# Performance work log

Hardware: AMD Instinct MI355X
Metric: run time of the kernel (lower is better)

## Reference

```python
import jax, jax.numpy as jnp
import numpy as np

B = 8192          # graphs
A = 1024          # atoms per graph
F = 32            # max fragments per graph
N = B * A
VIRTUAL_IDX = 4   # HPARAMS.get_node_idx('ligand_virtual')


def setup_inputs() -> dict:
    key = jax.random.key(0)
    k1, k2, k3, k4 = jax.random.split(key, 4)
    pos = jax.random.normal(k1, (N, 3), dtype=jnp.float32) * 10.0
    # -1 marks non-ligand atoms (no fragment), as in frag_idx_map semantics
    frag_idx_map = jax.random.randint(k2, (N,), -1, F, dtype=jnp.int32)
    batch_idx = (jnp.arange(N, dtype=jnp.int32) // A).astype(jnp.int32)
    node_entity = jax.random.randint(k3, (N,), 0, 6, dtype=jnp.int32)
    mask = jax.random.bernoulli(k4, 0.95, (N,))
    return {"pos": pos, "frag_idx_map": frag_idx_map, "batch_idx": batch_idx,
            "node_entity": node_entity, "mask": mask,
            "num_graphs": B, "max_frags_per_graph": F}


def reference(pos, frag_idx_map, batch_idx, node_entity, mask,
              num_graphs, max_frags_per_graph):
    """Fused equivalent of get_flat_fragment_index + get_fragment_com.

    Returns (coms [B*F, 3], counts [B*F], flat_frag_idx [N]).
    Rows of coms beyond a graph's actual fragment count are zero-padded.
    """
    Bn = num_graphs
    Fm = max_frags_per_graph
    is_ligand = frag_idx_map >= 0

    # num_frags_per_graph[i] = max(frag_idx in graph i) + 1 (0 if none)
    fmax = jax.ops.segment_max(jnp.where(is_ligand, frag_idx_map, -1),
                               batch_idx, num_segments=Bn)
    nfrag = jnp.maximum(fmax, -1) + 1  # [B]
    offset = jnp.concatenate([jnp.zeros((1,), nfrag.dtype),
                              jnp.cumsum(nfrag)[:-1]])  # [B]

    # flat fragment index in [0, sum(F_i)), -1 for non-ligand atoms
    flat_frag_idx = jnp.where(is_ligand,
                              frag_idx_map + offset[batch_idx],
                              -1)

    # COM excludes virtual nodes and masked dummies
    valid = is_ligand & mask & (node_entity != VIRTUAL_IDX)
    n_seg = Bn * Fm
    seg = jnp.where(valid, flat_frag_idx, n_seg)  # dump invalid into trash segment
    w = valid.astype(pos.dtype)
    sums = jax.ops.segment_sum(pos * w[:, None], seg, num_segments=n_seg + 1)[:-1]
    cnt = jax.ops.segment_sum(w, seg, num_segments=n_seg + 1)[:-1]
    coms = sums / jnp.maximum(cnt, 1.0)[:, None]
    return coms, cnt, flat_frag_idx
```

## Files before the change

kernel.cpp:

```cpp
#include <hip/hip_runtime.h>

#define GA 1024
#define GF 32
#define VIRT 4

typedef _Float16 half8 __attribute__((ext_vector_type(8)));
typedef float f32x4 __attribute__((ext_vector_type(4)));
typedef unsigned int uint4v __attribute__((ext_vector_type(4)));

#define XSTRIDE 2080
#define KOFF    (4 * XSTRIDE)
#define FOFF    (KOFF + GA)
#define LDSSZ   (FOFF + 4 * GF * 4 * 4)

__device__ __forceinline__ unsigned int h2(float a, float b) {
    const unsigned short lo = __builtin_bit_cast(unsigned short, (_Float16)a);
    const unsigned short hi = __builtin_bit_cast(unsigned short, (_Float16)b);
    return (unsigned int)lo | ((unsigned int)hi << 16);
}

__global__ __launch_bounds__(256) void k_graph_acc(
    const float* __restrict__ pos,
    const int*   __restrict__ frag,
    const int*   __restrict__ entity,
    const int*   __restrict__ mask,
    float*       __restrict__ sums_cnt,
    int*         __restrict__ nfrag)
{
    const int g    = blockIdx.x;
    const int t    = threadIdx.x;
    const int lane = t & 63;
    const int w    = t >> 6;

    __shared__ alignas(16) unsigned char lds[LDSSZ];
    __shared__ int s_wmax[4];

    const int i0 = g * GA + t * 4;
    const int4  f4 = *(const int4*)(frag   + i0);
    const int4  e4 = *(const int4*)(entity + i0);
    const int4  m4 = *(const int4*)(mask   + i0);
    const float4* p4 = (const float4*)(pos + (size_t)3 * i0);
    const float4 pa = p4[0], pb = p4[1], pc = p4[2];

    #define KEY(F,M,E) ((unsigned)(((F) >= 0 && (M) != 0 && (E) != VIRT) ? (unsigned)(F) : 0xFFu))
    const unsigned kp = KEY(f4.x,m4.x,e4.x)        | (KEY(f4.y,m4.y,e4.y) << 8)
                      | (KEY(f4.z,m4.z,e4.z) << 16) | (KEY(f4.w,m4.w,e4.w) << 24);
    *(unsigned*)(lds + KOFF + t * 4) = kp;
    #undef KEY

    *(uint2*)(lds + 0 * XSTRIDE + t * 8) = make_uint2(h2(pa.x, pa.w), h2(pb.z, pc.y));
    *(uint2*)(lds + 1 * XSTRIDE + t * 8) = make_uint2(h2(pa.y, pb.x), h2(pb.w, pc.z));
    *(uint2*)(lds + 2 * XSTRIDE + t * 8) = make_uint2(h2(pa.z, pb.y), h2(pc.x, pc.w));
    *(uint2*)(lds + 3 * XSTRIDE + t * 8) = make_uint2(0x3C003C00u, 0x3C003C00u);

    int lm = max(max(f4.x, f4.y), max(f4.z, f4.w));
    #pragma unroll
    for (int off = 32; off > 0; off >>= 1)
        lm = max(lm, __shfl_down(lm, off, 64));
    if (lane == 0) s_wmax[w] = lm;

    f32x4 acc0 = {0.f, 0.f, 0.f, 0.f};
    f32x4 acc1 = {0.f, 0.f, 0.f, 0.f};
    const int row = lane & 15;
    const int grp = lane >> 4;
    const unsigned xoff = (unsigned)((row & 3) * XSTRIDE + (w * 256 + grp * 8) * 2);
    const unsigned koff = (unsigned)(KOFF + w * 256 + grp * 8);

    #pragma unroll
    for (int s = 0; s < 8; ++s) {
        const uint2  kk = *(const uint2*)(lds + koff + s * 32);
        const uint4v bv = *(const uint4v*)(lds + xoff + s * 64);
        uint4v a0, a1;
        #pragma unroll
        for (int p = 0; p < 4; ++p) {
            const unsigned word = (p & 2) ? kk.y : kk.x;
            const unsigned k0 = (word >> ((p & 1) * 16)) & 0xFFu;
            const unsigned k1 = (word >> ((p & 1) * 16 + 8)) & 0xFFu;
            a0[p] = (k0 == (unsigned)row        ? 0x3C00u : 0u)
                  | (k1 == (unsigned)row        ? 0x3C000000u : 0u);
            a1[p] = (k0 == (unsigned)(row + 16) ? 0x3C00u : 0u)
                  | (k1 == (unsigned)(row + 16) ? 0x3C000000u : 0u);
        }
        acc0 = __builtin_amdgcn_mfma_f32_16x16x32_f16(
                   __builtin_bit_cast(half8, a0), __builtin_bit_cast(half8, bv), acc0, 0, 0, 0);
        acc1 = __builtin_amdgcn_mfma_f32_16x16x32_f16(
                   __builtin_bit_cast(half8, a1), __builtin_bit_cast(half8, bv), acc1, 0, 0, 0);
    }

    float* fold = (float*)(lds + FOFF);
    if (row < 4) {
        #pragma unroll
        for (int r = 0; r < 4; ++r) {
            fold[(w * GF + grp * 4 + r) * 4 + row]      = acc0[r];
            fold[(w * GF + 16 + grp * 4 + r) * 4 + row] = acc1[r];
        }
    }
    __syncthreads();
    if (t < GF * 4) {
        const float v = fold[t] + fold[128 + t] + fold[256 + t] + fold[384 + t];
        sums_cnt[(size_t)g * (GF * 4) + t] = v;
    }
    if (t == 0)
        nfrag[g] = max(max(s_wmax[0], s_wmax[1]), max(s_wmax[2], s_wmax[3])) + 1;
}

__global__ __launch_bounds__(256) void k_scan(
    const int* __restrict__ nfrag, int* __restrict__ offset, int B)
{
    const int t = threadIdx.x;
    const int C = B / 256;
    __shared__ int s[8192 + 256];
    __shared__ int ps[256];

    for (int k = 0; k < C; ++k) {
        const int idx = k * 256 + t;
        s[idx + (idx >> 5)] = nfrag[idx];
    }
    __syncthreads();

    int sum = 0;
    for (int k = 0; k < C; ++k) {
        const int idx = t * C + k;
        const int p = idx + (idx >> 5);
        const int v = s[p];
        s[p] = sum;
        sum += v;
    }
    ps[t] = sum;
    __syncthreads();

    for (int d = 1; d < 256; d <<= 1) {
        const int v = (t >= d) ? ps[t - d] : 0;
        __syncthreads();
        ps[t] += v;
        __syncthreads();
    }

    for (int k = 0; k < C; ++k) {
        const int idx = k * 256 + t;
        const int c = idx >> 5;
        const int pre = (c == 0) ? 0 : ps[c - 1];
        offset[idx] = pre + s[idx + (idx >> 5)];
    }
}

__global__ __launch_bounds__(256) void k_flat_fin(
    const int4*   __restrict__ frag4,
    const int*    __restrict__ offset,
    const int*    __restrict__ nfrag,
    const float4* __restrict__ sums_cnt,
    float*        __restrict__ coms,
    float*        __restrict__ cnt_out,
    float4*       __restrict__ out4,
    int B)
{
    const int b = blockIdx.x;
    const int t = threadIdx.x;
    const int i = b * 256 + t;
    const int off = offset[b];
    const int4 f = frag4[i];
    float4 o;
    o.x = (f.x >= 0) ? (float)(f.x + off) : -1.0f;
    o.y = (f.y >= 0) ? (float)(f.y + off) : -1.0f;
    o.z = (f.z >= 0) ? (float)(f.z + off) : -1.0f;
    o.w = (f.w >= 0) ? (float)(f.w + off) : -1.0f;
    out4[i] = o;

    if (b < (B * GF) / 256) {
        const int idx = b * 256 + t;
        const int g = idx >> 5;
        const int fr = idx & 31;
        if (fr < nfrag[g]) {
            const float4 s = sums_cnt[idx];
            const int rr = offset[g] + fr;
            const float inv = 1.0f / fmaxf(s.w, 1.0f);
            coms[3 * rr + 0] = s.x * inv;
            coms[3 * rr + 1] = s.y * inv;
            coms[3 * rr + 2] = s.z * inv;
            cnt_out[rr] = s.w;
        }
    }
}

extern "C" void kernel_launch(void* const* d_in, const int* in_sizes, int n_in,
                              void* d_out, int out_size, void* d_ws, size_t ws_size,
                              hipStream_t stream)
{
    const float* pos    = (const float*)d_in[0];
    const int*   frag   = (const int*)d_in[1];
    const int*   entity = (const int*)d_in[3];
    const int*   mask   = (const int*)d_in[4];

    const int N = in_sizes[1];
    const int B = N / GA;

    float* sums_cnt = (float*)d_ws;
    int*   nfrag    = (int*)(sums_cnt + (size_t)B * GF * 4);
    int*   offset   = nfrag + B;

    float* coms     = (float*)d_out;
    float* cnt_out  = coms + (size_t)B * GF * 3;
    float* flat_out = cnt_out + (size_t)B * GF;

    hipMemsetAsync(d_out, 0, (size_t)B * GF * 4 * sizeof(float), stream);

    k_graph_acc<<<B, 256, 0, stream>>>(pos, frag, entity, mask, sums_cnt, nfrag);
    k_scan<<<1, 256, 0, stream>>>(nfrag, offset, B);

    k_flat_fin<<<B, 256, 0, stream>>>(
        (const int4*)frag, offset, nfrag, (const float4*)sums_cnt,
        coms, cnt_out, (float4*)flat_out, B);
}
```

Baseline: 260.4 us.

## Process four graphs per block with register prefetch and double-buffered LDS

Each block of the accumulation kernel now handles four consecutive graphs instead of one. The next graph's inputs are loaded into registers while the current graph runs its LDS staging and MFMA reduction, and two LDS buffers alternate so that a single barrier per graph is enough. The aim is to hide global-load latency and cut block launch overhead; the kernel also gets a launch-bounds occupancy hint. The cost is higher register pressure and fewer blocks in flight, which lowers parallelism across the device.

```diff
diff --git a/kernel.cpp b/kernel.cpp
--- a/kernel.cpp
+++ b/kernel.cpp
@@ -3,6 +3,7 @@
 #define GA 1024
 #define GF 32
 #define VIRT 4
+#define NG 4
 
 typedef _Float16 half8 __attribute__((ext_vector_type(8)));
 typedef float f32x4 __attribute__((ext_vector_type(4)));
@@ -10,8 +11,9 @@
 
 #define XSTRIDE 2080
 #define KOFF    (4 * XSTRIDE)
-#define FOFF    (KOFF + GA)
-#define LDSSZ   (FOFF + 4 * GF * 4 * 4)
+#define BUFSZ   (KOFF + GA)
+#define FOLDOFF (3 * XSTRIDE)
+#define WMAXOFF (3 * XSTRIDE + 2048)
 
 __device__ __forceinline__ unsigned int h2(float a, float b) {
     const unsigned short lo = __builtin_bit_cast(unsigned short, (_Float16)a);
@@ -19,7 +21,7 @@
     return (unsigned int)lo | ((unsigned int)hi << 16);
 }
 
-__global__ __launch_bounds__(256) void k_graph_acc(
+__global__ __launch_bounds__(256, 6) void k_graph_acc(
     const float* __restrict__ pos,
     const int*   __restrict__ frag,
     const int*   __restrict__ entity,
@@ -27,81 +29,106 @@
     float*       __restrict__ sums_cnt,
     int*         __restrict__ nfrag)
 {
-    const int g    = blockIdx.x;
     const int t    = threadIdx.x;
     const int lane = t & 63;
     const int w    = t >> 6;
-
-    __shared__ alignas(16) unsigned char lds[LDSSZ];
-    __shared__ int s_wmax[4];
-
-    const int i0 = g * GA + t * 4;
-    const int4  f4 = *(const int4*)(frag   + i0);
-    const int4  e4 = *(const int4*)(entity + i0);
-    const int4  m4 = *(const int4*)(mask   + i0);
-    const float4* p4 = (const float4*)(pos + (size_t)3 * i0);
-    const float4 pa = p4[0], pb = p4[1], pc = p4[2];
-
-    #define KEY(F,M,E) ((unsigned)(((F) >= 0 && (M) != 0 && (E) != VIRT) ? (unsigned)(F) : 0xFFu))
-    const unsigned kp = KEY(f4.x,m4.x,e4.x)        | (KEY(f4.y,m4.y,e4.y) << 8)
-                      | (KEY(f4.z,m4.z,e4.z) << 16) | (KEY(f4.w,m4.w,e4.w) << 24);
-    *(unsigned*)(lds + KOFF + t * 4) = kp;
-    #undef KEY
-
-    *(uint2*)(lds + 0 * XSTRIDE + t * 8) = make_uint2(h2(pa.x, pa.w), h2(pb.z, pc.y));
-    *(uint2*)(lds + 1 * XSTRIDE + t * 8) = make_uint2(h2(pa.y, pb.x), h2(pb.w, pc.z));
-    *(uint2*)(lds + 2 * XSTRIDE + t * 8) = make_uint2(h2(pa.z, pb.y), h2(pc.x, pc.w));
-    *(uint2*)(lds + 3 * XSTRIDE + t * 8) = make_uint2(0x3C003C00u, 0x3C003C00u);
-
-    int lm = max(max(f4.x, f4.y), max(f4.z, f4.w));
-    #pragma unroll
-    for (int off = 32; off > 0; off >>= 1)
-        lm = max(lm, __shfl_down(lm, off, 64));
-    if (lane == 0) s_wmax[w] = lm;
-
-    f32x4 acc0 = {0.f, 0.f, 0.f, 0.f};
-    f32x4 acc1 = {0.f, 0.f, 0.f, 0.f};
+    const int g0   = blockIdx.x * NG;
+
+    __shared__ alignas(16) unsigned char lds[2 * BUFSZ];
+
     const int row = lane & 15;
     const int grp = lane >> 4;
-    const unsigned xoff = (unsigned)((row & 3) * XSTRIDE + (w * 256 + grp * 8) * 2);
-    const unsigned koff = (unsigned)(KOFF + w * 256 + grp * 8);
+    const unsigned xo_l = (unsigned)((row & 3) * XSTRIDE + (w * 256 + grp * 8) * 2);
+    const unsigned ko_l = (unsigned)(KOFF + w * 256 + grp * 8);
+
+    int4 f4, e4, m4; float4 pa, pb, pc;
+    {
+        const size_t i0 = (size_t)g0 * GA + t * 4;
+        f4 = *(const int4*)(frag   + i0);
+        e4 = *(const int4*)(entity + i0);
+        m4 = *(const int4*)(mask   + i0);
+        const float4* p4 = (const float4*)(pos + 3 * i0);
+        pa = p4[0]; pb = p4[1]; pc = p4[2];
+    }
 
     #pragma unroll
-    for (int s = 0; s < 8; ++s) {
-        const uint2  kk = *(const uint2*)(lds + koff + s * 32);
-        const uint4v bv = *(const uint4v*)(lds + xoff + s * 64);
-        uint4v a0, a1;
+    for (int it = 0; it < NG; ++it) {
+        unsigned char* buf = lds + (it & 1) * BUFSZ;
+
+        const int4  cf = f4, ce = e4, cm = m4;
+        const float4 qa = pa, qb = pb, qc = pc;
+
+        if (it + 1 < NG) {
+            const size_t i0 = (size_t)(g0 + it + 1) * GA + t * 4;
+            f4 = *(const int4*)(frag   + i0);
+            e4 = *(const int4*)(entity + i0);
+            m4 = *(const int4*)(mask   + i0);
+            const float4* p4 = (const float4*)(pos + 3 * i0);
+            pa = p4[0]; pb = p4[1]; pc = p4[2];
+        }
+
+        #define KEYV(F,M,E) ((unsigned)(((F) >= 0 && (M) != 0 && (E) != VIRT) ? (unsigned)(F) : 0xFFu))
+        const unsigned kp = KEYV(cf.x,cm.x,ce.x)        | (KEYV(cf.y,cm.y,ce.y) << 8)
+                          | (KEYV(cf.z,cm.z,ce.z) << 16) | (KEYV(cf.w,cm.w,ce.w) << 24);
+        *(unsigned*)(buf + KOFF + t * 4) = kp;
+        #undef KEYV
+        *(uint2*)(buf + 0 * XSTRIDE + t * 8) = make_uint2(h2(qa.x, qa.w), h2(qb.z, qc.y));
+        *(uint2*)(buf + 1 * XSTRIDE + t * 8) = make_uint2(h2(qa.y, qb.x), h2(qb.w, qc.z));
+        *(uint2*)(buf + 2 * XSTRIDE + t * 8) = make_uint2(h2(qa.z, qb.y), h2(qc.x, qc.w));
+        *(uint2*)(buf + 3 * XSTRIDE + t * 8) = make_uint2(0x3C003C00u, 0x3C003C00u);
+
+        int lm = max(max(cf.x, cf.y), max(cf.z, cf.w));
         #pragma unroll
-        for (int p = 0; p < 4; ++p) {
-            const unsigned word = (p & 2) ? kk.y : kk.x;
-            const unsigned k0 = (word >> ((p & 1) * 16)) & 0xFFu;
-            const unsigned k1 = (word >> ((p & 1) * 16 + 8)) & 0xFFu;
-            a0[p] = (k0 == (unsigned)row        ? 0x3C00u : 0u)
-                  | (k1 == (unsigned)row        ? 0x3C000000u : 0u);
-            a1[p] = (k0 == (unsigned)(row + 16) ? 0x3C00u : 0u)
-                  | (k1 == (unsigned)(row + 16) ? 0x3C000000u : 0u);
-        }
-        acc0 = __builtin_amdgcn_mfma_f32_16x16x32_f16(
-                   __builtin_bit_cast(half8, a0), __builtin_bit_cast(half8, bv), acc0, 0, 0, 0);
-        acc1 = __builtin_amdgcn_mfma_f32_16x16x32_f16(
-                   __builtin_bit_cast(half8, a1), __builtin_bit_cast(half8, bv), acc1, 0, 0, 0);
-    }
-
-    float* fold = (float*)(lds + FOFF);
-    if (row < 4) {
+        for (int off = 32; off > 0; off >>= 1)
+            lm = max(lm, __shfl_down(lm, off, 64));
+        if (lane == 0) *(int*)(buf + WMAXOFF + w * 4) = lm;
+
+        f32x4 acc0 = {0.f, 0.f, 0.f, 0.f};
+        f32x4 acc1 = {0.f, 0.f, 0.f, 0.f};
         #pragma unroll
-        for (int r = 0; r < 4; ++r) {
-            fold[(w * GF + grp * 4 + r) * 4 + row]      = acc0[r];
-            fold[(w * GF + 16 + grp * 4 + r) * 4 + row] = acc1[r];
-        }
-    }
-    __syncthreads();
-    if (t < GF * 4) {
-        const float v = fold[t] + fold[128 + t] + fold[256 + t] + fold[384 + t];
-        sums_cnt[(size_t)g * (GF * 4) + t] = v;
-    }
-    if (t == 0)
-        nfrag[g] = max(max(s_wmax[0], s_wmax[1]), max(s_wmax[2], s_wmax[3])) + 1;
+        for (int s = 0; s < 8; ++s) {
+            const uint2  kk = *(const uint2*)(buf + ko_l + s * 32);
+            const uint4v bv = *(const uint4v*)(buf + xo_l + s * 64);
+            uint4v a0, a1;
+            #pragma unroll
+            for (int p = 0; p < 4; ++p) {
+                const unsigned word = (p & 2) ? kk.y : kk.x;
+                const unsigned k0 = (word >> ((p & 1) * 16)) & 0xFFu;
+                const unsigned k1 = (word >> ((p & 1) * 16 + 8)) & 0xFFu;
+                a0[p] = (k0 == (unsigned)row        ? 0x3C00u : 0u)
+                      | (k1 == (unsigned)row        ? 0x3C000000u : 0u);
+                a1[p] = (k0 == (unsigned)(row + 16) ? 0x3C00u : 0u)
+                      | (k1 == (unsigned)(row + 16) ? 0x3C000000u : 0u);
+            }
+            acc0 = __builtin_amdgcn_mfma_f32_16x16x32_f16(
+                       __builtin_bit_cast(half8, a0), __builtin_bit_cast(half8, bv), acc0, 0, 0, 0);
+            acc1 = __builtin_amdgcn_mfma_f32_16x16x32_f16(
+                       __builtin_bit_cast(half8, a1), __builtin_bit_cast(half8, bv), acc1, 0, 0, 0);
+        }
+
+        float* fp = (float*)(buf + FOLDOFF + w * 512);
+        if (row < 4) {
+            #pragma unroll
+            for (int r = 0; r < 4; ++r) {
+                fp[(grp * 4 + r) * 4 + row]      = acc0[r];
+                fp[(16 + grp * 4 + r) * 4 + row] = acc1[r];
+            }
+        }
+
+        asm volatile("s_waitcnt lgkmcnt(0)" ::: "memory");
+        __builtin_amdgcn_s_barrier();
+        __builtin_amdgcn_sched_barrier(0);
+
+        if (t < 128) {
+            const float* f0 = (const float*)(buf + FOLDOFF);
+            const float v = f0[t] + f0[128 + t] + f0[256 + t] + f0[384 + t];
+            sums_cnt[(size_t)(g0 + it) * (GF * 4) + t] = v;
+        }
+        if (t == 0) {
+            const int* wm = (const int*)(buf + WMAXOFF);
+            nfrag[g0 + it] = max(max(wm[0], wm[1]), max(wm[2], wm[3])) + 1;
+        }
+    }
 }
 
 __global__ __launch_bounds__(256) void k_scan(
@@ -204,7 +231,7 @@
 
     hipMemsetAsync(d_out, 0, (size_t)B * GF * 4 * sizeof(float), stream);
 
-    k_graph_acc<<<B, 256, 0, stream>>>(pos, frag, entity, mask, sums_cnt, nfrag);
+    k_graph_acc<<<B / NG, 256, 0, stream>>>(pos, frag, entity, mask, sums_cnt, nfrag);
     k_scan<<<1, 256, 0, stream>>>(nfrag, offset, B);
 
     k_flat_fin<<<B, 256, 0, stream>>>(
```

Result: slower. 267.1 us (+2.6%).

## Fuse scan into finalize kernel, drop memset, compact fragment ids to bytes

Applied to the files above, without the earlier changes.

Removes the single-block scan kernel and the output memset. Each finalize block now recomputes the full prefix sum over per-graph fragment counts and zero-fills its own slice of the padded COM and count rows. The first kernel also writes fragment indices packed as bytes, so the flat-index pass reads a quarter of the original int bytes. Every one of the B/16 blocks repeats the 8192-entry scan, and the packed path depends on the workspace being large enough.

```diff
diff --git a/kernel.cpp b/kernel.cpp
--- a/kernel.cpp
+++ b/kernel.cpp
@@ -3,6 +3,7 @@
 #define GA 1024
 #define GF 32
 #define VIRT 4
+#define KG 16
 
 typedef _Float16 half8 __attribute__((ext_vector_type(8)));
 typedef float f32x4 __attribute__((ext_vector_type(4)));
@@ -25,7 +26,8 @@
     const int*   __restrict__ entity,
     const int*   __restrict__ mask,
     float*       __restrict__ sums_cnt,
-    int*         __restrict__ nfrag)
+    int*         __restrict__ nfrag,
+    unsigned*    __restrict__ frag8u)
 {
     const int g    = blockIdx.x;
     const int t    = threadIdx.x;
@@ -41,6 +43,12 @@
     const int4  m4 = *(const int4*)(mask   + i0);
     const float4* p4 = (const float4*)(pos + (size_t)3 * i0);
     const float4 pa = p4[0], pb = p4[1], pc = p4[2];
+
+    if (frag8u) {
+        const unsigned s8p = (f4.x & 0xFFu)         | ((f4.y & 0xFFu) << 8)
+                           | ((f4.z & 0xFFu) << 16) | ((unsigned)(f4.w & 0xFFu) << 24);
+        frag8u[(size_t)g * (GA / 4) + t] = s8p;
+    }
 
     #define KEY(F,M,E) ((unsigned)(((F) >= 0 && (M) != 0 && (E) != VIRT) ? (unsigned)(F) : 0xFFu))
     const unsigned kp = KEY(f4.x,m4.x,e4.x)        | (KEY(f4.y,m4.y,e4.y) << 8)
@@ -104,9 +112,17 @@
         nfrag[g] = max(max(s_wmax[0], s_wmax[1]), max(s_wmax[2], s_wmax[3])) + 1;
 }
 
-__global__ __launch_bounds__(256) void k_scan(
-    const int* __restrict__ nfrag, int* __restrict__ offset, int B)
+__global__ __launch_bounds__(256) void k_fin(
+    const int*      __restrict__ nfrag,
+    const float4*   __restrict__ sums_cnt,
+    const unsigned* __restrict__ frag8u,
+    const int4*     __restrict__ frag4,
+    float*          __restrict__ coms,
+    float*          __restrict__ cnt_out,
+    float4*         __restrict__ out4,
+    int B)
 {
+    const int b = blockIdx.x;
     const int t = threadIdx.x;
     const int C = B / 256;
     __shared__ int s[8192 + 256];
@@ -117,7 +133,6 @@
         s[idx + (idx >> 5)] = nfrag[idx];
     }
     __syncthreads();
-
     int sum = 0;
     for (int k = 0; k < C; ++k) {
         const int idx = t * C + k;
@@ -128,58 +143,66 @@
     }
     ps[t] = sum;
     __syncthreads();
-
     for (int d = 1; d < 256; d <<= 1) {
         const int v = (t >= d) ? ps[t - d] : 0;
         __syncthreads();
         ps[t] += v;
         __syncthreads();
     }
-
-    for (int k = 0; k < C; ++k) {
-        const int idx = k * 256 + t;
-        const int c = idx >> 5;
-        const int pre = (c == 0) ? 0 : ps[c - 1];
-        offset[idx] = pre + s[idx + (idx >> 5)];
-    }
-}
-
-__global__ __launch_bounds__(256) void k_flat_fin(
-    const int4*   __restrict__ frag4,
-    const int*    __restrict__ offset,
-    const int*    __restrict__ nfrag,
-    const float4* __restrict__ sums_cnt,
-    float*        __restrict__ coms,
-    float*        __restrict__ cnt_out,
-    float4*       __restrict__ out4,
-    int B)
-{
-    const int b = blockIdx.x;
-    const int t = threadIdx.x;
-    const int i = b * 256 + t;
-    const int off = offset[b];
-    const int4 f = frag4[i];
-    float4 o;
-    o.x = (f.x >= 0) ? (float)(f.x + off) : -1.0f;
-    o.y = (f.y >= 0) ? (float)(f.y + off) : -1.0f;
-    o.z = (f.z >= 0) ? (float)(f.z + off) : -1.0f;
-    o.w = (f.w >= 0) ? (float)(f.w + off) : -1.0f;
-    out4[i] = o;
-
-    if (b < (B * GF) / 256) {
-        const int idx = b * 256 + t;
-        const int g = idx >> 5;
-        const int fr = idx & 31;
+    #define OFF(g) (s[(g) + ((g) >> 5)] + (((g) >> 5) ? ps[((g) >> 5) - 1] : 0))
+    const int total = ps[255];
+
+    const int g0 = b * KG;
+
+    #pragma unroll
+    for (int k = 0; k < (KG * GF) / 256; ++k) {
+        const int e  = k * 256 + t;
+        const int j  = e >> 5, fr = e & 31;
+        const int g  = g0 + j;
         if (fr < nfrag[g]) {
-            const float4 s = sums_cnt[idx];
-            const int rr = offset[g] + fr;
-            const float inv = 1.0f / fmaxf(s.w, 1.0f);
-            coms[3 * rr + 0] = s.x * inv;
-            coms[3 * rr + 1] = s.y * inv;
-            coms[3 * rr + 2] = s.z * inv;
-            cnt_out[rr] = s.w;
-        }
-    }
+            const float4 v = sums_cnt[(size_t)g * GF + fr];
+            const int rr = OFF(g) + fr;
+            const float inv = 1.0f / fmaxf(v.w, 1.0f);
+            coms[3 * rr + 0] = v.x * inv;
+            coms[3 * rr + 1] = v.y * inv;
+            coms[3 * rr + 2] = v.z * inv;
+            cnt_out[rr] = v.w;
+        }
+    }
+
+    #pragma unroll
+    for (int k = 0; k < 2; ++k) {
+        const int r = b * 512 + k * 256 + t;
+        if (r >= total) {
+            coms[3 * r + 0] = 0.0f; coms[3 * r + 1] = 0.0f; coms[3 * r + 2] = 0.0f;
+            cnt_out[r] = 0.0f;
+        }
+    }
+
+    for (int j = 0; j < KG; ++j) {
+        const int g = g0 + j;
+        const float fo = (float)OFF(g);
+        float4 o;
+        if (frag8u) {
+            const unsigned kk = frag8u[(size_t)g * (GA / 4) + t];
+            const int a0 = ((int)(kk << 24)) >> 24;
+            const int a1 = ((int)(kk << 16)) >> 24;
+            const int a2 = ((int)(kk <<  8)) >> 24;
+            const int a3 = ((int)kk) >> 24;
+            o.x = (a0 >= 0) ? (float)a0 + fo : -1.0f;
+            o.y = (a1 >= 0) ? (float)a1 + fo : -1.0f;
+            o.z = (a2 >= 0) ? (float)a2 + fo : -1.0f;
+            o.w = (a3 >= 0) ? (float)a3 + fo : -1.0f;
+        } else {
+            const int4 f = frag4[(size_t)g * (GA / 4) + t];
+            o.x = (f.x >= 0) ? (float)f.x + fo : -1.0f;
+            o.y = (f.y >= 0) ? (float)f.y + fo : -1.0f;
+            o.z = (f.z >= 0) ? (float)f.z + fo : -1.0f;
+            o.w = (f.w >= 0) ? (float)f.w + fo : -1.0f;
+        }
+        out4[(size_t)g * (GA / 4) + t] = o;
+    }
+    #undef OFF
 }
 
 extern "C" void kernel_launch(void* const* d_in, const int* in_sizes, int n_in,
@@ -194,20 +217,19 @@
     const int N = in_sizes[1];
     const int B = N / GA;
 
-    float* sums_cnt = (float*)d_ws;
-    int*   nfrag    = (int*)(sums_cnt + (size_t)B * GF * 4);
-    int*   offset   = nfrag + B;
+    float*    sums_cnt = (float*)d_ws;
+    int*      nfrag    = (int*)(sums_cnt + (size_t)B * GF * 4);
+    unsigned* frag8u   = (unsigned*)(nfrag + B);
+    const size_t needed = (size_t)B * GF * 4 * 4 + (size_t)B * 4 + (size_t)N;
+    if (ws_size < needed) frag8u = nullptr;
 
     float* coms     = (float*)d_out;
     float* cnt_out  = coms + (size_t)B * GF * 3;
     float* flat_out = cnt_out + (size_t)B * GF;
 
-    hipMemsetAsync(d_out, 0, (size_t)B * GF * 4 * sizeof(float), stream);
-
-    k_graph_acc<<<B, 256, 0, stream>>>(pos, frag, entity, mask, sums_cnt, nfrag);
-    k_scan<<<1, 256, 0, stream>>>(nfrag, offset, B);
-
-    k_flat_fin<<<B, 256, 0, stream>>>(
-        (const int4*)frag, offset, nfrag, (const float4*)sums_cnt,
+    k_graph_acc<<<B, 256, 0, stream>>>(pos, frag, entity, mask, sums_cnt, nfrag, frag8u);
+
+    k_fin<<<B / KG, 256, 0, stream>>>(
+        nfrag, (const float4*)sums_cnt, (const unsigned*)frag8u, (const int4*)frag,
         coms, cnt_out, (float4*)flat_out, B);
 }
```

Measured after the change: 259.8 us. About the same (-0.2%).
